# Kernel optimization log

Measured on AMD Instinct MI355X. Metric: run time of the kernel, lower is better.

## Reference

```python
import jax, jax.numpy as jnp
import numpy as np

LATENT, D_MODEL, WIN, ENC_IN, BATCH = 128, 512, 256, 55, 256


def setup_inputs() -> dict:
    key = jax.random.key(0)
    ks = jax.random.split(key, 9)
    sl = lambda k, shape, fan_in: (jax.random.normal(k, shape, jnp.float32) / np.sqrt(fan_in)).astype(jnp.float32)
    return {
        "z": jax.random.normal(ks[0], (BATCH, LATENT), jnp.float32),
        "h_proj_w": sl(ks[1], (D_MODEL, LATENT), LATENT),
        "h_proj_b": sl(ks[2], (D_MODEL,), LATENT),
        "w_ih": sl(ks[3], (3 * D_MODEL, D_MODEL), D_MODEL),
        "w_hh": sl(ks[4], (3 * D_MODEL, D_MODEL), D_MODEL),
        "b_ih": sl(ks[5], (3 * D_MODEL,), D_MODEL),
        "b_hh": sl(ks[6], (3 * D_MODEL,), D_MODEL),
        "out_w": sl(ks[7], (ENC_IN, D_MODEL), D_MODEL),
        "out_b": sl(ks[8], (ENC_IN,), D_MODEL),
        "win_size": WIN,
    }


def reference(z, h_proj_w, h_proj_b, w_ih, w_hh, b_ih, b_hh, out_w, out_b, win_size):
    d = h_proj_w.shape[0]
    # h0 = tanh(Linear(z)) -> [B, d]
    h0 = jnp.tanh(z @ h_proj_w.T + h_proj_b)
    # GRU input is all zeros, so input-gate preactivation is just b_ih
    # (w_ih @ 0 == 0); gate order in torch GRU is (r, z, n).
    gi_r, gi_z, gi_n = b_ih[:d], b_ih[d:2 * d], b_ih[2 * d:]

    def step(h, _):
        gh = h @ w_hh.T + b_hh                      # [B, 3d]
        r = jax.nn.sigmoid(gi_r + gh[:, :d])
        zg = jax.nn.sigmoid(gi_z + gh[:, d:2 * d])
        n = jnp.tanh(gi_n + r * gh[:, 2 * d:])
        h_new = (1.0 - zg) * n + zg * h
        return h_new, h_new

    _, hs = jax.lax.scan(step, h0, None, length=win_size)  # [T, B, d]
    hs = jnp.transpose(hs, (1, 0, 2))                      # [B, T, d]
    return hs @ out_w.T + out_b                            # [B, T, enc_in]
```

## Files before the change

kernel.cpp:

```cpp
#include <hip/hip_runtime.h>

#define DM     512
#define LAT    128
#define WIN_   256
#define ENC    55
#define GB     32
#define BT     8
#define DS     64
#define TPB    768
#define OUT_T  256
#define AROWB  1056
#define GHS    200
#define OWS    520

typedef __attribute__((ext_vector_type(8))) short bf8;
typedef __attribute__((ext_vector_type(4))) float f4;
typedef unsigned long long u64;
typedef unsigned short u16;

__device__ __align__(128) u64 g_ring[2 * 256 * 128];
__device__ __align__(128) u64 g_flag[GB * 8 * 16];

__device__ __forceinline__ u16 f2bf(float f) {
    union { float f; unsigned int i; } v; v.f = f;
    unsigned int r = v.i + 0x7fffu + ((v.i >> 16) & 1u);
    return (u16)(r >> 16);
}
__device__ __forceinline__ u64 pack4(float a, float b, float c, float d) {
    return (u64)f2bf(a) | ((u64)f2bf(b) << 16) | ((u64)f2bf(c) << 32) | ((u64)f2bf(d) << 48);
}
__device__ __forceinline__ float sigm(float x) { return 1.f / (1.f + __expf(-x)); }
__device__ __forceinline__ float tanh_(float x) {
    x = fminf(x, 40.f);
    float e = __expf(2.f * x);
    return (e - 1.f) / (e + 1.f);
}
#define ALOAD(p)     __hip_atomic_load((p),      __ATOMIC_RELAXED, __HIP_MEMORY_SCOPE_AGENT)
#define ASTORE(p, v) __hip_atomic_store((p), (v), __ATOMIC_RELAXED, __HIP_MEMORY_SCOPE_AGENT)

__global__ __launch_bounds__(TPB, 3) void gru_fused(
    const float* __restrict__ z,
    const float* __restrict__ hpw,
    const float* __restrict__ hpb,
    const float* __restrict__ whh,
    const float* __restrict__ bih,
    const float* __restrict__ bhh,
    const float* __restrict__ outw,
    const float* __restrict__ outb,
    float* __restrict__ out)
{
    const int blk  = blockIdx.x;
    const int g    = blk & (GB - 1);
    const int s    = blk >> 5;
    const int d0   = s * DS;
    const int row0 = g * BT;
    const int tid  = threadIdx.x;
    const int wave = tid >> 6;
    const int lane = tid & 63;
    const int quad = lane >> 4;
    const int nl   = lane & 15;

    __shared__ __align__(16) unsigned char smemA[BT * AROWB];
    __shared__ __align__(16) float ghT[BT][GHS];
    __shared__ float bias_r[DS], bias_z[DS], gin_[DS], bhn_[DS];
    __shared__ __align__(16) float hprev[BT][DS];
    __shared__ __align__(16) float h0tmp[BT][DS];
    __shared__ __align__(16) u16 sOutW[ENC * OWS];
    __shared__ float sOutB[64];
    __shared__ u64 sh_base;

    u64* flag_own = g_flag + (u64)(g * 8 + s) * 16;
    if (tid == 0) sh_base = ALOAD(flag_own);

    if (tid < DS) {
        int dg = d0 + tid;
        bias_r[tid] = bih[dg]       + bhh[dg];
        bias_z[tid] = bih[512 + dg] + bhh[512 + dg];
        gin_[tid]   = bih[1024 + dg];
        bhn_[tid]   = bhh[1024 + dg];
    }
    if (tid < ENC) sOutB[tid] = outb[tid];
    for (int i = tid; i < ENC * DM; i += TPB)
        sOutW[(i >> 9) * OWS + (i & 511)] = f2bf(outw[i]);

    const int gl   = wave * 16 + nl;
    const int sel  = gl >> 6;
    const int jrow = sel * 512 + d0 + (gl & 63);
    bf8 bfrag[16];
#pragma unroll
    for (int kb = 0; kb < 16; ++kb) {
        const float* wp = whh + jrow * DM + kb * 32 + quad * 8;
        bf8 v;
#pragma unroll
        for (int j = 0; j < 8; ++j) v[j] = (short)f2bf(wp[j]);
        bfrag[kb] = v;
    }

    if (tid < BT * DS) {
        int d = tid & (DS - 1), bl = tid >> 6;
        float acc = hpb[d0 + d];
        const float* zr = z + (row0 + bl) * LAT;
        const float* wr = hpw + (d0 + d) * LAT;
#pragma unroll 8
        for (int k = 0; k < LAT; ++k) acc += zr[k] * wr[k];
        h0tmp[bl][d] = tanh_(acc);
    }
    __syncthreads();

    const u64 base = sh_base;
    const int prow = lane >> 3;
    const int pdc  = (lane & 7) * 8;
    u64 pk0 = 0, pk1 = 0;

    if (wave == 0) {
        const float* hv = &h0tmp[prow][pdc];
        pk0 = pack4(hv[0], hv[1], hv[2], hv[3]);
        pk1 = pack4(hv[4], hv[5], hv[6], hv[7]);
        *(f4*)&hprev[prow][pdc]     = *(const f4*)&h0tmp[prow][pdc];
        *(f4*)&hprev[prow][pdc + 4] = *(const f4*)&h0tmp[prow][pdc + 4];
        u64* dst = g_ring + (u64)(row0 + prow) * 128 + (d0 >> 2) + (lane & 7) * 2;
        ASTORE(dst, pk0);
        ASTORE(dst + 1, pk1);
        asm volatile("s_waitcnt vmcnt(0)" ::: "memory");
        if (lane == 0) ASTORE(flag_own, base + 1);
    }

    const char* afrag_p = (const char*)smemA + (nl & 7) * AROWB + quad * 16;

    for (int t = 1; t <= WIN_; ++t) {
        const int sp = (t - 1) & 1, sc = t & 1;

        if (wave == 0) {
            char* dp = (char*)smemA + prow * AROWB + (d0 + pdc) * 2;
            *(u64*)dp = pk0; *(u64*)(dp + 8) = pk1;
        } else if (wave < 8) {
            const int j = (s + wave) & 7;
            u64* fp = g_flag + (u64)(g * 8 + j) * 16;
            const u64 want = base + t;
            long guard = 0;
            while (ALOAD(fp) < want && guard < (1L << 20)) ++guard;
            asm volatile("" ::: "memory");
            const u64* src = g_ring + (u64)(sp * 256 + row0 + prow) * 128
                             + j * 16 + (lane & 7) * 2;
            u64 lo = ALOAD(src), hi = ALOAD(src + 1);
            char* dp = (char*)smemA + prow * AROWB + j * 128 + (lane & 7) * 16;
            *(u64*)dp = lo; *(u64*)(dp + 8) = hi;
        }
        __syncthreads();

        f4 acc = {0.f, 0.f, 0.f, 0.f};
#pragma unroll
        for (int kb = 0; kb < 16; ++kb) {
            bf8 av = *(const bf8*)(afrag_p + kb * 64);
            acc = __builtin_amdgcn_mfma_f32_16x16x32_bf16(av, bfrag[kb], acc, 0, 0, 0);
        }
        if (quad < 2) {
            const int c = sel * 64 + (gl & 63);
#pragma unroll
            for (int r = 0; r < 4; ++r) ghT[quad * 4 + r][c] = acc[r];
        }
        __syncthreads();

        if (wave == 0) {
            const float* grow = &ghT[prow][0];
            f4 hp0 = *(const f4*)&hprev[prow][pdc];
            f4 hp1 = *(const f4*)&hprev[prow][pdc + 4];
            float hn[8];
#pragma unroll
            for (int j = 0; j < 8; ++j) {
                int d = pdc + j;
                float rr = sigm(bias_r[d] + grow[d]);
                float zg = sigm(bias_z[d] + grow[64 + d]);
                float nn = tanh_(gin_[d] + rr * (bhn_[d] + grow[128 + d]));
                float hpj = (j < 4) ? hp0[j] : hp1[j - 4];
                hn[j] = (1.f - zg) * nn + zg * hpj;
            }
            pk0 = pack4(hn[0], hn[1], hn[2], hn[3]);
            pk1 = pack4(hn[4], hn[5], hn[6], hn[7]);
            f4 w0 = {hn[0], hn[1], hn[2], hn[3]}, w1 = {hn[4], hn[5], hn[6], hn[7]};
            *(f4*)&hprev[prow][pdc] = w0;
            *(f4*)&hprev[prow][pdc + 4] = w1;
            u64* dst = g_ring + (u64)(sc * 256 + row0 + prow) * 128 + (d0 >> 2) + (lane & 7) * 2;
            ASTORE(dst, pk0);
            ASTORE(dst + 1, pk1);
            asm volatile("s_waitcnt vmcnt(0)" ::: "memory");
            if (lane == 0) ASTORE(flag_own, base + 1 + t);
        }

        const int tau = t - 2;
        const bool proj = (tau >= 0) && ((tau & 7) == s);
        if (proj && wave >= 8) {
            const int e  = (wave - 8) * 16 + nl;
            const int ec = (e < ENC) ? e : (ENC - 1);
            const u16* wrow = sOutW + ec * OWS + quad * 8;
            f4 accp = {0.f, 0.f, 0.f, 0.f};
#pragma unroll
            for (int kb = 0; kb < 16; ++kb) {
                bf8 av = *(const bf8*)(afrag_p + kb * 64);
                bf8 wv = *(const bf8*)(wrow + kb * 32);
                accp = __builtin_amdgcn_mfma_f32_16x16x32_bf16(av, wv, accp, 0, 0, 0);
            }
            if (quad < 2 && e < ENC) {
                float ob = sOutB[e];
#pragma unroll
                for (int r = 0; r < 4; ++r) {
                    int m = quad * 4 + r;
                    out[(row0 + m) * (OUT_T * ENC) + tau * ENC + e] = accp[r] + ob;
                }
            }
        }
        if (proj) __syncthreads();
    }

    if (s == 7) {
        if (wave == 0) {
            char* dp = (char*)smemA + prow * AROWB + (d0 + pdc) * 2;
            *(u64*)dp = pk0; *(u64*)(dp + 8) = pk1;
        } else if (wave < 8) {
            const int j = (s + wave) & 7;
            u64* fp = g_flag + (u64)(g * 8 + j) * 16;
            const u64 want = base + 1 + WIN_;
            long guard = 0;
            while (ALOAD(fp) < want && guard < (1L << 20)) ++guard;
            asm volatile("" ::: "memory");
            const u64* src = g_ring + (u64)(row0 + prow) * 128 + j * 16 + (lane & 7) * 2;
            u64 lo = ALOAD(src), hi = ALOAD(src + 1);
            char* dp = (char*)smemA + prow * AROWB + j * 128 + (lane & 7) * 16;
            *(u64*)dp = lo; *(u64*)(dp + 8) = hi;
        }
        __syncthreads();
        if (wave >= 8) {
            const int e  = (wave - 8) * 16 + nl;
            const int ec = (e < ENC) ? e : (ENC - 1);
            const u16* wrow = sOutW + ec * OWS + quad * 8;
            f4 accp = {0.f, 0.f, 0.f, 0.f};
#pragma unroll
            for (int kb = 0; kb < 16; ++kb) {
                bf8 av = *(const bf8*)(afrag_p + kb * 64);
                bf8 wv = *(const bf8*)(wrow + kb * 32);
                accp = __builtin_amdgcn_mfma_f32_16x16x32_bf16(av, wv, accp, 0, 0, 0);
            }
            if (quad < 2 && e < ENC) {
                float ob = sOutB[e];
#pragma unroll
                for (int r = 0; r < 4; ++r) {
                    int m = quad * 4 + r;
                    out[(row0 + m) * (OUT_T * ENC) + 255 * ENC + e] = accp[r] + ob;
                }
            }
        }
    }
}

extern "C" void kernel_launch(void* const* d_in, const int* in_sizes, int n_in,
                              void* d_out, int out_size, void* d_ws, size_t ws_size,
                              hipStream_t stream) {
    const float* z    = (const float*)d_in[0];
    const float* hpw  = (const float*)d_in[1];
    const float* hpb  = (const float*)d_in[2];
    const float* whh  = (const float*)d_in[4];
    const float* bih  = (const float*)d_in[5];
    const float* bhh  = (const float*)d_in[6];
    const float* outw = (const float*)d_in[7];
    const float* outb = (const float*)d_in[8];
    float* out = (float*)d_out;

    (void)d_ws; (void)ws_size;
    gru_fused<<<dim3(256), dim3(TPB), 0, stream>>>(
        z, hpw, hpb, whh, bih, bhh, outw, outb, out);
}
```

Baseline: 863.9 us.

## Replace flag-based GRU step sync with sequence-tagged ring records

Each 64-bit ring record now carries a 16-bit sequence tag plus three bf16 hidden values. Consumers poll the data words directly until every lane sees the expected tag, so the separate flag store, the vmcnt(0) wait before signalling, and the dependent flag-then-data load chain all go away. The hidden state now lives in registers instead of a shared hprev buffer, and a per-launch counter replaces the monotonic flag as the base for sequence numbers. The cost is more records per row (22 instead of 16), unaligned 3-element packing with scalar LDS stores, and reliance on 64-bit atomic stores never being seen torn.

```diff
diff --git a/kernel.cpp b/kernel.cpp
--- a/kernel.cpp
+++ b/kernel.cpp
@@ -9,25 +9,24 @@
 #define DS     64
 #define TPB    768
 #define OUT_T  256
-#define AROWB  1056
+#define AROW16 528
 #define GHS    200
 #define OWS    520
+#define NK     22
+#define NKP    24
 
 typedef __attribute__((ext_vector_type(8))) short bf8;
 typedef __attribute__((ext_vector_type(4))) float f4;
 typedef unsigned long long u64;
 typedef unsigned short u16;
 
-__device__ __align__(128) u64 g_ring[2 * 256 * 128];
-__device__ __align__(128) u64 g_flag[GB * 8 * 16];
+__device__ __align__(128) u64 g_ring2[2][GB][8][BT][NKP];
+__device__ __align__(128) u64 g_lcnt[GB * 8 * 16];
 
 __device__ __forceinline__ u16 f2bf(float f) {
     union { float f; unsigned int i; } v; v.f = f;
     unsigned int r = v.i + 0x7fffu + ((v.i >> 16) & 1u);
     return (u16)(r >> 16);
-}
-__device__ __forceinline__ u64 pack4(float a, float b, float c, float d) {
-    return (u64)f2bf(a) | ((u64)f2bf(b) << 16) | ((u64)f2bf(c) << 32) | ((u64)f2bf(d) << 48);
 }
 __device__ __forceinline__ float sigm(float x) { return 1.f / (1.f + __expf(-x)); }
 __device__ __forceinline__ float tanh_(float x) {
@@ -60,17 +59,16 @@
     const int quad = lane >> 4;
     const int nl   = lane & 15;
 
-    __shared__ __align__(16) unsigned char smemA[BT * AROWB];
+    __shared__ __align__(16) u16 sm16[BT * AROW16];
     __shared__ __align__(16) float ghT[BT][GHS];
     __shared__ float bias_r[DS], bias_z[DS], gin_[DS], bhn_[DS];
-    __shared__ __align__(16) float hprev[BT][DS];
     __shared__ __align__(16) float h0tmp[BT][DS];
     __shared__ __align__(16) u16 sOutW[ENC * OWS];
     __shared__ float sOutB[64];
     __shared__ u64 sh_base;
 
-    u64* flag_own = g_flag + (u64)(g * 8 + s) * 16;
-    if (tid == 0) sh_base = ALOAD(flag_own);
+    u64* lc_own = g_lcnt + (u64)(g * 8 + s) * 16;
+    if (tid == 0) sh_base = ALOAD(lc_own) * 512ULL;
 
     if (tid < DS) {
         int dg = d0 + tid;
@@ -109,49 +107,81 @@
 
     const u64 base = sh_base;
     const int prow = lane >> 3;
-    const int pdc  = (lane & 7) * 8;
-    u64 pk0 = 0, pk1 = 0;
-
+    const int kc   = lane & 7;
+
+    float hreg[3][3];
     if (wave == 0) {
-        const float* hv = &h0tmp[prow][pdc];
-        pk0 = pack4(hv[0], hv[1], hv[2], hv[3]);
-        pk1 = pack4(hv[4], hv[5], hv[6], hv[7]);
-        *(f4*)&hprev[prow][pdc]     = *(const f4*)&h0tmp[prow][pdc];
-        *(f4*)&hprev[prow][pdc + 4] = *(const f4*)&h0tmp[prow][pdc + 4];
-        u64* dst = g_ring + (u64)(row0 + prow) * 128 + (d0 >> 2) + (lane & 7) * 2;
-        ASTORE(dst, pk0);
-        ASTORE(dst + 1, pk1);
-        asm volatile("s_waitcnt vmcnt(0)" ::: "memory");
-        if (lane == 0) ASTORE(flag_own, base + 1);
-    }
-
-    const char* afrag_p = (const char*)smemA + (nl & 7) * AROWB + quad * 16;
+#pragma unroll
+        for (int m = 0; m < 3; ++m) {
+            int k = kc + 8 * m;
+#pragma unroll
+            for (int i = 0; i < 3; ++i) {
+                int d = 3 * k + i;
+                hreg[m][i] = (k < NK && d < DS) ? h0tmp[prow][d] : 0.f;
+            }
+        }
+        const u16 sq = (u16)base;
+#pragma unroll
+        for (int m = 0; m < 3; ++m) {
+            int k = kc + 8 * m;
+            if (k < NK) {
+                u64 rec = (u64)sq | ((u64)f2bf(hreg[m][0]) << 16) |
+                          ((u64)f2bf(hreg[m][1]) << 32) | ((u64)f2bf(hreg[m][2]) << 48);
+                ASTORE(&g_ring2[0][g][s][prow][k], rec);
+            }
+        }
+    }
+
+    const u16* afrag_base = sm16 + (nl & 7) * AROW16;
 
     for (int t = 1; t <= WIN_; ++t) {
         const int sp = (t - 1) & 1, sc = t & 1;
+        const u16 want = (u16)(base + t - 1);
 
         if (wave == 0) {
-            char* dp = (char*)smemA + prow * AROWB + (d0 + pdc) * 2;
-            *(u64*)dp = pk0; *(u64*)(dp + 8) = pk1;
+#pragma unroll
+            for (int m = 0; m < 3; ++m) {
+                int k = kc + 8 * m;
+#pragma unroll
+                for (int i = 0; i < 3; ++i) {
+                    int d = 3 * k + i;
+                    if (k < NK && d < DS) sm16[prow * AROW16 + d0 + d] = f2bf(hreg[m][i]);
+                }
+            }
         } else if (wave < 8) {
             const int j = (s + wave) & 7;
-            u64* fp = g_flag + (u64)(g * 8 + j) * 16;
-            const u64 want = base + t;
+            u64* p0 = &g_ring2[sp][g][j][prow][kc];
+            u64 r0, r1, r2;
             long guard = 0;
-            while (ALOAD(fp) < want && guard < (1L << 20)) ++guard;
-            asm volatile("" ::: "memory");
-            const u64* src = g_ring + (u64)(sp * 256 + row0 + prow) * 128
-                             + j * 16 + (lane & 7) * 2;
-            u64 lo = ALOAD(src), hi = ALOAD(src + 1);
-            char* dp = (char*)smemA + prow * AROWB + j * 128 + (lane & 7) * 16;
-            *(u64*)dp = lo; *(u64*)(dp + 8) = hi;
+            const bool v2 = (kc + 16) < NK;
+            for (;;) {
+                r0 = ALOAD(p0);
+                r1 = ALOAD(p0 + 8);
+                r2 = v2 ? ALOAD(p0 + 16) : 0;
+                bool ok = ((u16)r0 == want) && ((u16)r1 == want) &&
+                          (!v2 || (u16)r2 == want);
+                if (__all(ok) || ++guard > (1L << 20)) break;
+            }
+            u16* dst = sm16 + prow * AROW16 + j * 64;
+            {
+                int db = 3 * kc;
+                dst[db] = (u16)(r0 >> 16); dst[db + 1] = (u16)(r0 >> 32); dst[db + 2] = (u16)(r0 >> 48);
+                db = 3 * (kc + 8);
+                dst[db] = (u16)(r1 >> 16); dst[db + 1] = (u16)(r1 >> 32); dst[db + 2] = (u16)(r1 >> 48);
+                if (v2) {
+                    db = 3 * (kc + 16);
+                    dst[db] = (u16)(r2 >> 16);
+                    if (db + 1 < DS) dst[db + 1] = (u16)(r2 >> 32);
+                    if (db + 2 < DS) dst[db + 2] = (u16)(r2 >> 48);
+                }
+            }
         }
         __syncthreads();
 
         f4 acc = {0.f, 0.f, 0.f, 0.f};
 #pragma unroll
         for (int kb = 0; kb < 16; ++kb) {
-            bf8 av = *(const bf8*)(afrag_p + kb * 64);
+            bf8 av = *(const bf8*)(afrag_base + quad * 8 + kb * 32);
             acc = __builtin_amdgcn_mfma_f32_16x16x32_bf16(av, bfrag[kb], acc, 0, 0, 0);
         }
         if (quad < 2) {
@@ -163,28 +193,28 @@
 
         if (wave == 0) {
             const float* grow = &ghT[prow][0];
-            f4 hp0 = *(const f4*)&hprev[prow][pdc];
-            f4 hp1 = *(const f4*)&hprev[prow][pdc + 4];
-            float hn[8];
-#pragma unroll
-            for (int j = 0; j < 8; ++j) {
-                int d = pdc + j;
-                float rr = sigm(bias_r[d] + grow[d]);
-                float zg = sigm(bias_z[d] + grow[64 + d]);
-                float nn = tanh_(gin_[d] + rr * (bhn_[d] + grow[128 + d]));
-                float hpj = (j < 4) ? hp0[j] : hp1[j - 4];
-                hn[j] = (1.f - zg) * nn + zg * hpj;
-            }
-            pk0 = pack4(hn[0], hn[1], hn[2], hn[3]);
-            pk1 = pack4(hn[4], hn[5], hn[6], hn[7]);
-            f4 w0 = {hn[0], hn[1], hn[2], hn[3]}, w1 = {hn[4], hn[5], hn[6], hn[7]};
-            *(f4*)&hprev[prow][pdc] = w0;
-            *(f4*)&hprev[prow][pdc + 4] = w1;
-            u64* dst = g_ring + (u64)(sc * 256 + row0 + prow) * 128 + (d0 >> 2) + (lane & 7) * 2;
-            ASTORE(dst, pk0);
-            ASTORE(dst + 1, pk1);
-            asm volatile("s_waitcnt vmcnt(0)" ::: "memory");
-            if (lane == 0) ASTORE(flag_own, base + 1 + t);
+            const u16 sq = (u16)(base + t);
+#pragma unroll
+            for (int m = 0; m < 3; ++m) {
+                int k = kc + 8 * m;
+                if (k < NK) {
+                    u16 b[3] = {0, 0, 0};
+#pragma unroll
+                    for (int i = 0; i < 3; ++i) {
+                        int d = 3 * k + i;
+                        if (d < DS) {
+                            float rr = sigm(bias_r[d] + grow[d]);
+                            float zg = sigm(bias_z[d] + grow[64 + d]);
+                            float nn = tanh_(gin_[d] + rr * (bhn_[d] + grow[128 + d]));
+                            float h  = (1.f - zg) * nn + zg * hreg[m][i];
+                            hreg[m][i] = h;
+                            b[i] = f2bf(h);
+                        }
+                    }
+                    u64 rec = (u64)sq | ((u64)b[0] << 16) | ((u64)b[1] << 32) | ((u64)b[2] << 48);
+                    ASTORE(&g_ring2[sc][g][s][prow][k], rec);
+                }
+            }
         }
 
         const int tau = t - 2;
@@ -196,7 +226,7 @@
             f4 accp = {0.f, 0.f, 0.f, 0.f};
 #pragma unroll
             for (int kb = 0; kb < 16; ++kb) {
-                bf8 av = *(const bf8*)(afrag_p + kb * 64);
+                bf8 av = *(const bf8*)(afrag_base + quad * 8 + kb * 32);
                 bf8 wv = *(const bf8*)(wrow + kb * 32);
                 accp = __builtin_amdgcn_mfma_f32_16x16x32_bf16(av, wv, accp, 0, 0, 0);
             }
@@ -213,20 +243,42 @@
     }
 
     if (s == 7) {
+        const u16 want = (u16)(base + WIN_);
         if (wave == 0) {
-            char* dp = (char*)smemA + prow * AROWB + (d0 + pdc) * 2;
-            *(u64*)dp = pk0; *(u64*)(dp + 8) = pk1;
+#pragma unroll
+            for (int m = 0; m < 3; ++m) {
+                int k = kc + 8 * m;
+#pragma unroll
+                for (int i = 0; i < 3; ++i) {
+                    int d = 3 * k + i;
+                    if (k < NK && d < DS) sm16[prow * AROW16 + d0 + d] = f2bf(hreg[m][i]);
+                }
+            }
         } else if (wave < 8) {
             const int j = (s + wave) & 7;
-            u64* fp = g_flag + (u64)(g * 8 + j) * 16;
-            const u64 want = base + 1 + WIN_;
+            u64* p0 = &g_ring2[0][g][j][prow][kc];
+            u64 r0, r1, r2;
             long guard = 0;
-            while (ALOAD(fp) < want && guard < (1L << 20)) ++guard;
-            asm volatile("" ::: "memory");
-            const u64* src = g_ring + (u64)(row0 + prow) * 128 + j * 16 + (lane & 7) * 2;
-            u64 lo = ALOAD(src), hi = ALOAD(src + 1);
-            char* dp = (char*)smemA + prow * AROWB + j * 128 + (lane & 7) * 16;
-            *(u64*)dp = lo; *(u64*)(dp + 8) = hi;
+            const bool v2 = (kc + 16) < NK;
+            for (;;) {
+                r0 = ALOAD(p0);
+                r1 = ALOAD(p0 + 8);
+                r2 = v2 ? ALOAD(p0 + 16) : 0;
+                bool ok = ((u16)r0 == want) && ((u16)r1 == want) &&
+                          (!v2 || (u16)r2 == want);
+                if (__all(ok) || ++guard > (1L << 20)) break;
+            }
+            u16* dst = sm16 + prow * AROW16 + j * 64;
+            int db = 3 * kc;
+            dst[db] = (u16)(r0 >> 16); dst[db + 1] = (u16)(r0 >> 32); dst[db + 2] = (u16)(r0 >> 48);
+            db = 3 * (kc + 8);
+            dst[db] = (u16)(r1 >> 16); dst[db + 1] = (u16)(r1 >> 32); dst[db + 2] = (u16)(r1 >> 48);
+            if (v2) {
+                db = 3 * (kc + 16);
+                dst[db] = (u16)(r2 >> 16);
+                if (db + 1 < DS) dst[db + 1] = (u16)(r2 >> 32);
+                if (db + 2 < DS) dst[db + 2] = (u16)(r2 >> 48);
+            }
         }
         __syncthreads();
         if (wave >= 8) {
@@ -236,7 +288,7 @@
             f4 accp = {0.f, 0.f, 0.f, 0.f};
 #pragma unroll
             for (int kb = 0; kb < 16; ++kb) {
-                bf8 av = *(const bf8*)(afrag_p + kb * 64);
+                bf8 av = *(const bf8*)(afrag_base + quad * 8 + kb * 32);
                 bf8 wv = *(const bf8*)(wrow + kb * 32);
                 accp = __builtin_amdgcn_mfma_f32_16x16x32_bf16(av, wv, accp, 0, 0, 0);
             }
@@ -250,6 +302,9 @@
             }
         }
     }
+
+    __syncthreads();
+    if (tid == 0) ASTORE(lc_own, (base / 512ULL) + 1ULL);
 }
 
 extern "C" void kernel_launch(void* const* d_in, const int* in_sizes, int n_in,
```

New measurement: 1.225 ms. +41.8%, slower.
